# Kernel optimization log

Measured on AMD Instinct MI355X. Metric: run time of the kernel, lower is better.

Reference implementation:

```python
import jax, jax.numpy as jnp
import numpy as np

B, N, K, C, DK, DV, H, W = 16, 5, 5, 512, 128, 128, 16, 16

def setup_inputs() -> dict:
    key = jax.random.key(0)
    k1, k2, k3, k4 = jax.random.split(key, 4)
    return {
        "query_repr": jax.random.normal(k1, (B, C, H, W), dtype=jnp.float32),
        "supports_repr": jax.random.normal(k2, (B, N, K, C, H, W), dtype=jnp.float32),
        "w_qk": jax.random.normal(k3, (DK, C), dtype=jnp.float32) * (C ** -0.5),
        "w_v": jax.random.normal(k4, (DV, C), dtype=jnp.float32) * (C ** -0.5),
    }

def reference(query_repr, supports_repr, w_qk, w_v):
    scale = DK ** -0.5
    # 1x1 convs == per-pixel linear projections
    query_q = jnp.einsum('oc,bchw->bohw', w_qk, query_repr)          # [b,dk,h,w]
    query_v = jnp.einsum('oc,bchw->bohw', w_v, query_repr)           # [b,dv,h,w]
    supports_k = jnp.einsum('oc,bnkchw->bnkohw', w_qk, supports_repr)  # [b,n,k,dk,h,w]
    supports_v = jnp.einsum('oc,bnkchw->bnkohw', w_v, supports_repr)   # [b,n,k,dv,h,w]

    # attention: query pixel (h,w) attends over all support pixels (k,i,j)
    sim = jnp.einsum('bchw,bnkcij->bnhwkij', query_q, supports_k) * scale
    b, n, h, w = sim.shape[:4]
    attn = jax.nn.softmax(sim.reshape(b, n, h, w, -1), axis=-1)
    attn = attn.reshape(b, n, h, w, K, h, w)
    out = jnp.einsum('bnhwkij,bnkcij->bnchw', attn, supports_v)      # [b,n,dv,h,w]

    out = out.reshape(b, n, -1)                                      # [b,n,dv*h*w]
    qv = query_v.reshape(b, 1, -1)                                   # [b,1,dv*h*w]
    euclidean_dist = jnp.sum((qv - out) ** 2, axis=-1) / (h * w)     # [b,n]
    return -euclidean_dist
```

## Files before the change

kernel.cpp:

```cpp
#include <hip/hip_runtime.h>
#include <hip/hip_bf16.h>
#include <stdint.h>

constexpr int Bv = 16, Nv = 5, Kv = 5, Cv = 512, DKv = 128, DVv = 128, HWv = 256;
constexpr int NSUP = Bv * Nv * Kv;
constexpr int NSLAB = NSUP + Bv;

typedef __attribute__((ext_vector_type(8))) short bf16x8;
typedef __attribute__((ext_vector_type(4))) float f32x4;

static __device__ __forceinline__ unsigned short f2b(float x) {
  __hip_bfloat16 h = __float2bfloat16(x);
  return *reinterpret_cast<unsigned short*>(&h);
}

#define SB0() __builtin_amdgcn_sched_barrier(0)
#define BARRIER() __builtin_amdgcn_s_barrier()
#define WAITVM(N) asm volatile("s_waitcnt vmcnt(" #N ")" ::: "memory")
#define WAITLGKM0() asm volatile("s_waitcnt lgkmcnt(0)" ::: "memory")

__global__ __launch_bounds__(256) void prep_kernel(
    const float* __restrict__ query, const float* __restrict__ w_qk,
    const float* __restrict__ w_v, unsigned short* __restrict__ WbF,
    unsigned short* __restrict__ Xb, float* __restrict__ out, int out_n) {
  __shared__ unsigned short lds[64][68];
  const int bid = blockIdx.x;
  const int tid = threadIdx.x;
  if (bid < 64) {
    int gidx = bid * 256 + tid;
    int l = gidx & 63;
    int nb = (gidx >> 6) & 7;
    int ks = (gidx >> 9) & 1;
    int kt = (gidx >> 10) & 7;
    int h = (gidx >> 13) & 1;
    int row = nb * 16 + (l & 15);
    int c0 = kt * 64 + ks * 32 + (l >> 4) * 8;
    const float* src = (h ? w_v : w_qk) + (size_t)row * Cv + c0;
    float4 a = *(const float4*)src;
    float4 b = *(const float4*)(src + 4);
    union { unsigned short u[8]; uint4 v; } t;
    t.u[0] = f2b(a.x); t.u[1] = f2b(a.y); t.u[2] = f2b(a.z); t.u[3] = f2b(a.w);
    t.u[4] = f2b(b.x); t.u[5] = f2b(b.y); t.u[6] = f2b(b.z); t.u[7] = f2b(b.w);
    *(uint4*)(WbF + (size_t)gidx * 8) = t.v;
  } else if (bid < 576) {
    const int blk = bid - 64;
    const int s = NSUP + (blk >> 5);
    const int tq = blk & 31;
    const int cb = tq >> 2, pb = tq & 3;
    const int c0 = cb * 64, p0 = pb * 64;
    const float* __restrict__ X = query + (size_t)(s - NSUP) * Cv * HWv;
#pragma unroll
    for (int r = 0; r < 4; ++r) {
      int cl = (tid >> 4) + r * 16;
      int pl = (tid & 15) * 4;
      float4 v = *(const float4*)(X + (size_t)(c0 + cl) * HWv + p0 + pl);
      ushort4 u;
      u.x = f2b(v.x); u.y = f2b(v.y); u.z = f2b(v.z); u.w = f2b(v.w);
      *(ushort4*)&lds[cl][pl] = u;
    }
    __syncthreads();
    const int pl2 = tid >> 2;
    const int q0 = (tid & 3) * 16;
    union { unsigned short u[16]; uint4 v4[2]; } tmp;
#pragma unroll
    for (int jj = 0; jj < 16; ++jj) {
      int j = (jj + pl2) & 15;
      tmp.u[j] = lds[q0 + j][pl2];
    }
    unsigned short* dst = Xb + ((size_t)s * HWv + p0 + pl2) * Cv + c0 + q0;
    *(uint4*)dst = tmp.v4[0];
    *((uint4*)dst + 1) = tmp.v4[1];
  } else {
    if (tid < out_n) out[tid] = 0.0f;
  }
}

__global__ __launch_bounds__(256, 3) void proj_all_kernel(
    const float* __restrict__ supports, const unsigned short* __restrict__ WbF,
    unsigned short* __restrict__ KbF, unsigned short* __restrict__ VbF,
    const unsigned short* __restrict__ Xb, unsigned short* __restrict__ Qb,
    float* __restrict__ QVf) {
  __shared__ __align__(16) char smem[49152];
  const int bid = blockIdx.x;
  const int t = threadIdx.x;
  const int lane = t & 63, wid = t >> 6;
  const int wr = wid >> 1, wc = wid & 1;
  const int l15 = lane & 15, g = lane >> 4;

  f32x4 acc[2][8] = {};

  if (bid < 1600) {
    const int s = bid >> 2;
    const int pixq = bid & 3;
    float* F0 = (float*)smem;
    float* F1 = (float*)(smem + 16384);
    unsigned short* X0 = (unsigned short*)(smem + 32768);
    unsigned short* X1 = (unsigned short*)(smem + 40960);
    const float* __restrict__ Xs = supports + (size_t)s * Cv * HWv + pixq * 64;

    auto dma = [&](int kt, float* dstF) {
#pragma unroll
      for (int i = 0; i < 4; ++i) {
        const int seg = wid * 4 + i;
        const float* gsrc =
            Xs + (size_t)(kt * 64 + seg * 4 + (lane >> 4)) * HWv + (lane & 15) * 4;
        __builtin_amdgcn_global_load_lds(
            (const __attribute__((address_space(1))) void*)gsrc,
            (__attribute__((address_space(3))) void*)((char*)dstF + seg * 1024),
            16, 0, 0);
      }
    };
    auto stageB = [&](const float* srcF, unsigned short* dstX) {
#pragma unroll
      for (int h2 = 0; h2 < 2; ++h2) {
        const int sidx = h2 * 256 + t;
        const int sslot = sidx >> 6;
        const int row = sidx & 63;
        union { unsigned short u[8]; uint4 q; } pk;
#pragma unroll
        for (int j = 0; j < 8; ++j)
          pk.u[j] = f2b(srcF[(size_t)(sslot * 8 + j) * 64 + row]);
        *(uint4*)((char*)dstX + row * 128 + ((sslot ^ (row & 7)) * 16)) = pk.q;
      }
    };

    dma(0, F0);
    dma(1, F1);
    SB0(); WAITVM(4); SB0(); BARRIER(); SB0();
    stageB(F0, X0);
    WAITLGKM0(); SB0(); BARRIER(); SB0();

    for (int kt = 0; kt < 8; ++kt) {
      const int cur = kt & 1;
      float* Fc = cur ? F1 : F0;
      const unsigned short* Xc = cur ? X1 : X0;
      if (kt < 6) dma(kt + 2, Fc);
#pragma unroll
      for (int ks = 0; ks < 2; ++ks) {
        const int sx = ((ks * 4 + g) ^ (l15 & 7)) * 16;
        bf16x8 A[2], Bf[8];
#pragma unroll
        for (int m = 0; m < 2; ++m)
          A[m] = *(const bf16x8*)((const char*)Xc + (wr * 32 + m * 16 + l15) * 128 + sx);
#pragma unroll
        for (int n = 0; n < 8; ++n) {
          const int h = n >> 2;
          const int nb = wc * 4 + (n & 3);
          Bf[n] = *(const bf16x8*)(
              WbF + (size_t)((((h * 8 + kt) * 2 + ks) * 8 + nb) * 64 + lane) * 8);
        }
#pragma unroll
        for (int m = 0; m < 2; ++m)
#pragma unroll
          for (int n = 0; n < 8; ++n)
            acc[m][n] = __builtin_amdgcn_mfma_f32_16x16x32_bf16(A[m], Bf[n],
                                                                acc[m][n], 0, 0, 0);
      }
      if (kt < 7) {
        SB0();
        if (kt < 6) { WAITVM(4); } else { WAITVM(0); }
        SB0(); BARRIER(); SB0();
        float* Fn = cur ? F0 : F1;
        unsigned short* Xn = cur ? X0 : X1;
        stageB(Fn, Xn);
        WAITLGKM0(); SB0(); BARRIER(); SB0();
      }
    }

    unsigned short* bounce = (unsigned short*)smem;
#pragma unroll
    for (int m = 0; m < 2; ++m) {
      const int pr = wr * 32 + m * 16 + g * 4;
#pragma unroll
      for (int n = 0; n < 4; ++n) {
        const int dk = wc * 64 + n * 16 + l15;
#pragma unroll
        for (int r = 0; r < 4; ++r)
          bounce[(size_t)(pr + r) * 140 + dk] = f2b(acc[m][n][r]);
      }
    }
    __syncthreads();
    {
      unsigned short* Kdst = KbF + ((size_t)s * 4 + pixq) * 8192;
#pragma unroll
      for (int i = 0; i < 4; ++i) {
        const int u = i * 256 + t;
        const int jl15 = u & 15, jg = (u >> 4) & 3, jkc = (u >> 6) & 3,
                  jnc = (u >> 8) & 3;
        const int pixl = jnc * 16 + jl15;
        const int dk = jkc * 32 + jg * 8;
        *(uint4*)(Kdst + (size_t)u * 8) = *(const uint4*)(bounce + (size_t)pixl * 140 + dk);
      }
    }
    __syncthreads();
#pragma unroll
    for (int m = 0; m < 2; ++m) {
      const int pr = wr * 32 + m * 16 + g * 4;
#pragma unroll
      for (int n = 0; n < 4; ++n) {
        const int dv = wc * 64 + n * 16 + l15;
#pragma unroll
        for (int r = 0; r < 4; ++r)
          bounce[(size_t)dv * 72 + pr + r] = f2b(acc[m][4 + n][r]);
      }
    }
    __syncthreads();
    {
      unsigned short* Vdst = VbF + ((size_t)s * 4 + pixq) * 8192;
#pragma unroll
      for (int i = 0; i < 4; ++i) {
        const int u = i * 256 + t;
        const int jl15 = u & 15, jg = (u >> 4) & 3, jd = (u >> 6) & 7,
                  jkc2 = (u >> 9) & 1;
        const int dv = jd * 16 + jl15;
        const int nsl = jkc2 * 32 + jg * 8;
        *(uint4*)(Vdst + (size_t)u * 8) = *(const uint4*)(bounce + (size_t)dv * 72 + nsl);
      }
    }
  } else {
    const int r0 = bid - 1600;
    const int sq = r0 >> 2;
    const int pixq = r0 & 3;
    unsigned short* Xt2 = (unsigned short*)smem;
    const unsigned short* __restrict__ Xq =
        Xb + ((size_t)(NSUP + sq) * HWv + pixq * 64) * Cv;

    auto dmaQ = [&](int kt, int buf) {
#pragma unroll
      for (int i = 0; i < 2; ++i) {
        const int seg = wid * 2 + i;
        const int row = seg * 8 + (lane >> 3);
        const int srcslot = (lane & 7) ^ ((lane >> 3) & 7);
        const unsigned short* gsrc = Xq + (size_t)row * Cv + kt * 64 + srcslot * 8;
        __builtin_amdgcn_global_load_lds(
            (const __attribute__((address_space(1))) void*)gsrc,
            (__attribute__((address_space(3))) void*)((char*)Xt2 + buf * 8192 + seg * 1024),
            16, 0, 0);
      }
    };

    dmaQ(0, 0);
    dmaQ(1, 1);
    SB0(); WAITVM(2); SB0(); BARRIER(); SB0();
    for (int kt = 0; kt < 8; ++kt) {
      if (kt < 6) dmaQ(kt + 2, (kt + 2) & 3);
      const char* Xt = (const char*)Xt2 + (kt & 3) * 8192;
#pragma unroll
      for (int ks = 0; ks < 2; ++ks) {
        const int sx = ((ks * 4 + g) ^ (l15 & 7)) * 16;
        bf16x8 A[2], Bf[8];
#pragma unroll
        for (int m = 0; m < 2; ++m)
          A[m] = *(const bf16x8*)(Xt + (wr * 32 + m * 16 + l15) * 128 + sx);
#pragma unroll
        for (int n = 0; n < 8; ++n) {
          const int h = n >> 2;
          const int nb = wc * 4 + (n & 3);
          Bf[n] = *(const bf16x8*)(
              WbF + (size_t)((((h * 8 + kt) * 2 + ks) * 8 + nb) * 64 + lane) * 8);
        }
#pragma unroll
        for (int m = 0; m < 2; ++m)
#pragma unroll
          for (int n = 0; n < 8; ++n)
            acc[m][n] = __builtin_amdgcn_mfma_f32_16x16x32_bf16(A[m], Bf[n],
                                                                acc[m][n], 0, 0, 0);
      }
      if (kt < 7) {
        SB0();
        if (kt < 6) { WAITVM(2); } else { WAITVM(0); }
        SB0(); BARRIER(); SB0();
      }
    }

#pragma unroll
    for (int m = 0; m < 2; ++m) {
      const int pixr = pixq * 64 + wr * 32 + m * 16 + g * 4;
#pragma unroll
      for (int n = 0; n < 4; ++n) {
        const int oc = wc * 64 + n * 16 + l15;
        unsigned short* p = Qb + ((size_t)sq * HWv + pixr) * DKv + oc;
#pragma unroll
        for (int r = 0; r < 4; ++r) p[(size_t)r * DKv] = f2b(acc[m][n][r]);
      }
#pragma unroll
      for (int n = 0; n < 4; ++n) {
        const int oc = wc * 64 + n * 16 + l15;
        float* p = QVf + ((size_t)sq * HWv + pixr) * DVv + oc;
#pragma unroll
        for (int r = 0; r < 4; ++r) p[(size_t)r * DVv] = acc[m][4 + n][r];
      }
    }
  }
}

__global__ __launch_bounds__(256) void attn_mfma_kernel(
    const unsigned short* __restrict__ KbF, const unsigned short* __restrict__ VbF,
    const unsigned short* __restrict__ Qb, const float* __restrict__ QVf,
    float* __restrict__ out) {
  __shared__ __align__(16) char smem[74784];
  unsigned short* Klds = (unsigned short*)smem;
  unsigned short* Vlds = (unsigned short*)(smem + 32768);
  unsigned short* Plds = (unsigned short*)(smem + 65536);
  float* redbuf = (float*)(smem + 74752);

  const int L = blockIdx.x;
  const int bid = (L & 7) * 40 + (L >> 3);
  const int bn = bid >> 2, qh = bid & 3;
  const int b = bn / Nv;
  const int t = threadIdx.x;
  const int l = t & 63, wid = t >> 6;
  const int l15 = l & 15, g = l >> 4;
  const int qpix0 = qh * 64 + wid * 16;
  constexpr float C2 = 0.08838834764831845f * 1.4426950408889634f;

  bf16x8 qa[4];
#pragma unroll
  for (int kc = 0; kc < 4; ++kc)
    qa[kc] = *(const bf16x8*)(
        Qb + ((size_t)(b * HWv + qpix0 + l15)) * DKv + kc * 32 + g * 8);

  f32x4 oacc[8] = {};
  float mrow[4], lrow[4];
#pragma unroll
  for (int r = 0; r < 4; ++r) { mrow[r] = -3e38f; lrow[r] = 0.0f; }

  unsigned short* Pw = Plds + wid * 16 * 72;

  auto dma = [&](int c, int buf) {
    const int s2 = bn * Kv + (c >> 2);
    const int chunk = c & 3;
    const unsigned short* Kc = KbF + ((size_t)s2 * 4 + chunk) * 8192;
    const unsigned short* Vc = VbF + ((size_t)s2 * 4 + chunk) * 8192;
#pragma unroll
    for (int i = 0; i < 4; ++i) {
      const int seg = wid * 4 + i;
      __builtin_amdgcn_global_load_lds(
          (const __attribute__((address_space(1))) void*)(Kc + (size_t)(seg * 64 + l) * 8),
          (__attribute__((address_space(3))) void*)(Klds + (size_t)buf * 8192 + seg * 512),
          16, 0, 0);
      __builtin_amdgcn_global_load_lds(
          (const __attribute__((address_space(1))) void*)(Vc + (size_t)(seg * 64 + l) * 8),
          (__attribute__((address_space(3))) void*)(Vlds + (size_t)buf * 8192 + seg * 512),
          16, 0, 0);
    }
  };

  dma(0, 0);
  __syncthreads();
  for (int c = 0; c < 20; ++c) {
    const int cur = c & 1;
    if (c < 19) dma(c + 1, cur ^ 1);
    const unsigned short* Kc = Klds + (size_t)cur * 8192;
    const unsigned short* Vc = Vlds + (size_t)cur * 8192;

    f32x4 s4[4];
#pragma unroll
    for (int nc = 0; nc < 4; ++nc) {
      f32x4 sv = {};
#pragma unroll
      for (int kc = 0; kc < 4; ++kc) {
        bf16x8 kf = *(const bf16x8*)(Kc + (size_t)((nc * 4 + kc) * 64 + l) * 8);
        sv = __builtin_amdgcn_mfma_f32_16x16x32_bf16(qa[kc], kf, sv, 0, 0, 0);
      }
      s4[nc] = sv;
    }
    float pm[4];
#pragma unroll
    for (int r = 0; r < 4; ++r) {
      float v = s4[0][r];
#pragma unroll
      for (int nc = 1; nc < 4; ++nc) v = fmaxf(v, s4[nc][r]);
      pm[r] = v;
    }
#pragma unroll
    for (int off = 1; off <= 8; off <<= 1)
#pragma unroll
      for (int r = 0; r < 4; ++r) pm[r] = fmaxf(pm[r], __shfl_xor(pm[r], off));
    float sc[4];
#pragma unroll
    for (int r = 0; r < 4; ++r) {
      float mn = fmaxf(mrow[r], pm[r]);
      sc[r] = exp2f(C2 * (mrow[r] - mn));
      mrow[r] = mn;
      lrow[r] *= sc[r];
    }
#pragma unroll
    for (int d = 0; d < 8; ++d)
#pragma unroll
      for (int r = 0; r < 4; ++r) oacc[d][r] *= sc[r];
#pragma unroll
    for (int nc = 0; nc < 4; ++nc)
#pragma unroll
      for (int r = 0; r < 4; ++r) {
        float p = exp2f(C2 * (s4[nc][r] - mrow[r]));
        lrow[r] += p;
        Pw[(size_t)(g * 4 + r) * 72 + nc * 16 + l15] = f2b(p);
      }
#pragma unroll
    for (int kc2 = 0; kc2 < 2; ++kc2) {
      bf16x8 pa = *(const bf16x8*)(Pw + (size_t)l15 * 72 + kc2 * 32 + g * 8);
#pragma unroll
      for (int d = 0; d < 8; ++d) {
        bf16x8 vf = *(const bf16x8*)(Vc + (size_t)((kc2 * 8 + d) * 64 + l) * 8);
        oacc[d] = __builtin_amdgcn_mfma_f32_16x16x32_bf16(pa, vf, oacc[d], 0, 0, 0);
      }
    }
    __syncthreads();
  }

#pragma unroll
  for (int off = 1; off <= 8; off <<= 1)
#pragma unroll
    for (int r = 0; r < 4; ++r) lrow[r] += __shfl_xor(lrow[r], off);
  float linv[4];
#pragma unroll
  for (int r = 0; r < 4; ++r) linv[r] = 1.0f / lrow[r];

  float part = 0.0f;
#pragma unroll
  for (int d = 0; d < 8; ++d)
#pragma unroll
    for (int r = 0; r < 4; ++r) {
      float o = oacc[d][r] * linv[r];
      float qv = QVf[((size_t)(b * HWv + qpix0 + g * 4 + r)) * DVv + d * 16 + l15];
      float df = qv - o;
      part += df * df;
    }
#pragma unroll
  for (int off = 1; off <= 32; off <<= 1) part += __shfl_xor(part, off);
  if (l == 0) redbuf[wid] = part;
  __syncthreads();
  if (t == 0) {
    float tot = redbuf[0] + redbuf[1] + redbuf[2] + redbuf[3];
    atomicAdd(out + bn, -tot * (1.0f / HWv));
  }
}

extern "C" void kernel_launch(void* const* d_in, const int* in_sizes, int n_in,
                              void* d_out, int out_size, void* d_ws, size_t ws_size,
                              hipStream_t stream) {
  const float* query = (const float*)d_in[0];
  const float* supports = (const float*)d_in[1];
  const float* w_qk = (const float*)d_in[2];
  const float* w_v = (const float*)d_in[3];
  float* out = (float*)d_out;

  const size_t sz_kb = (size_t)NSUP * 4 * 8192 * 2;
  const size_t sz_vb = (size_t)NSUP * 4 * 8192 * 2;
  const size_t sz_qb = (size_t)Bv * HWv * DKv * 2;
  const size_t sz_qvf = (size_t)Bv * HWv * DVv * 4;
  const size_t sz_xb = (size_t)NSLAB * HWv * Cv * 2;
  const size_t sz_wb = (size_t)256 * Cv * 2;

  char* p = (char*)d_ws;
  unsigned short* KbF = (unsigned short*)p;           p += sz_kb;
  unsigned short* VbF = (unsigned short*)p;           p += sz_vb;
  unsigned short* Qb = (unsigned short*)p;            p += sz_qb;
  float* QVf = (float*)p;                             p += sz_qvf;
  unsigned short* Xb = (unsigned short*)p;            p += sz_xb;
  p += sz_wb;
  unsigned short* WbF = (unsigned short*)p;

  prep_kernel<<<577, 256, 0, stream>>>(query, w_qk, w_v, WbF, Xb, out, out_size);
  proj_all_kernel<<<1664, 256, 0, stream>>>(supports, WbF, KbF, VbF, Xb, Qb, QVf);
  attn_mfma_kernel<<<Bv * Nv * 4, 256, 0, stream>>>(KbF, VbF, Qb, QVf, out);
}
```

Measured before the change: 152.8 us.

## Stage support tiles through registers and repartition waves by output head

The support projection path drops the async global-to-LDS fp32 staging buffers. Each thread now loads its fp32 values into registers one k-tile ahead, converts them to bf16 and writes them directly into the swizzled LDS tile, which cuts LDS from 48KB to 32KB. The wave split also changes: each wave now covers all 64 pixels for one head (K or V) and half of the channels, so every B fragment load feeds more MFMAs. The costs are more registers for the prefetched values, and simple vmcnt(0) waits in the query path that may expose load latency.

```diff
diff --git a/kernel.cpp b/kernel.cpp
--- a/kernel.cpp
+++ b/kernel.cpp
@@ -16,7 +16,6 @@
 
 #define SB0() __builtin_amdgcn_sched_barrier(0)
 #define BARRIER() __builtin_amdgcn_s_barrier()
-#define WAITVM(N) asm volatile("s_waitcnt vmcnt(" #N ")" ::: "memory")
 #define WAITLGKM0() asm volatile("s_waitcnt lgkmcnt(0)" ::: "memory")
 
 __global__ __launch_bounds__(256) void prep_kernel(
@@ -80,103 +79,91 @@
     unsigned short* __restrict__ KbF, unsigned short* __restrict__ VbF,
     const unsigned short* __restrict__ Xb, unsigned short* __restrict__ Qb,
     float* __restrict__ QVf) {
-  __shared__ __align__(16) char smem[49152];
+  __shared__ __align__(16) char smem[32768];
   const int bid = blockIdx.x;
   const int t = threadIdx.x;
   const int lane = t & 63, wid = t >> 6;
-  const int wr = wid >> 1, wc = wid & 1;
+  const int wc = wid & 3;
+  const int hsel = wc >> 1;
+  const int nq = wc & 1;
   const int l15 = lane & 15, g = lane >> 4;
 
-  f32x4 acc[2][8] = {};
+  f32x4 acc[4][4] = {};
 
   if (bid < 1600) {
     const int s = bid >> 2;
     const int pixq = bid & 3;
-    float* F0 = (float*)smem;
-    float* F1 = (float*)(smem + 16384);
-    unsigned short* X0 = (unsigned short*)(smem + 32768);
-    unsigned short* X1 = (unsigned short*)(smem + 40960);
+    unsigned short* X0 = (unsigned short*)smem;
+    unsigned short* X1 = (unsigned short*)(smem + 8192);
     const float* __restrict__ Xs = supports + (size_t)s * Cv * HWv + pixq * 64;
-
-    auto dma = [&](int kt, float* dstF) {
-#pragma unroll
-      for (int i = 0; i < 4; ++i) {
-        const int seg = wid * 4 + i;
-        const float* gsrc =
-            Xs + (size_t)(kt * 64 + seg * 4 + (lane >> 4)) * HWv + (lane & 15) * 4;
-        __builtin_amdgcn_global_load_lds(
-            (const __attribute__((address_space(1))) void*)gsrc,
-            (__attribute__((address_space(3))) void*)((char*)dstF + seg * 1024),
-            16, 0, 0);
-      }
+    const int slot0 = wid, slot1 = wid + 4;
+
+    float fst[16];
+    auto aload = [&](int kt) {
+#pragma unroll
+      for (int j = 0; j < 8; ++j)
+        fst[j] = Xs[(size_t)(kt * 64 + slot0 * 8 + j) * HWv + lane];
+#pragma unroll
+      for (int j = 0; j < 8; ++j)
+        fst[8 + j] = Xs[(size_t)(kt * 64 + slot1 * 8 + j) * HWv + lane];
     };
-    auto stageB = [&](const float* srcF, unsigned short* dstX) {
-#pragma unroll
-      for (int h2 = 0; h2 < 2; ++h2) {
-        const int sidx = h2 * 256 + t;
-        const int sslot = sidx >> 6;
-        const int row = sidx & 63;
-        union { unsigned short u[8]; uint4 q; } pk;
-#pragma unroll
-        for (int j = 0; j < 8; ++j)
-          pk.u[j] = f2b(srcF[(size_t)(sslot * 8 + j) * 64 + row]);
-        *(uint4*)((char*)dstX + row * 128 + ((sslot ^ (row & 7)) * 16)) = pk.q;
-      }
+    auto awrite = [&](unsigned short* dstX) {
+      union { unsigned short u[8]; uint4 q; } pk;
+#pragma unroll
+      for (int j = 0; j < 8; ++j) pk.u[j] = f2b(fst[j]);
+      *(uint4*)((char*)dstX + lane * 128 + ((slot0 ^ (lane & 7)) * 16)) = pk.q;
+#pragma unroll
+      for (int j = 0; j < 8; ++j) pk.u[j] = f2b(fst[8 + j]);
+      *(uint4*)((char*)dstX + lane * 128 + ((slot1 ^ (lane & 7)) * 16)) = pk.q;
     };
 
-    dma(0, F0);
-    dma(1, F1);
-    SB0(); WAITVM(4); SB0(); BARRIER(); SB0();
-    stageB(F0, X0);
+    aload(0);
+    awrite(X0);
     WAITLGKM0(); SB0(); BARRIER(); SB0();
 
     for (int kt = 0; kt < 8; ++kt) {
       const int cur = kt & 1;
-      float* Fc = cur ? F1 : F0;
       const unsigned short* Xc = cur ? X1 : X0;
-      if (kt < 6) dma(kt + 2, Fc);
+      unsigned short* Xn = cur ? X0 : X1;
+      if (kt < 7) aload(kt + 1);
+      SB0();
 #pragma unroll
       for (int ks = 0; ks < 2; ++ks) {
         const int sx = ((ks * 4 + g) ^ (l15 & 7)) * 16;
-        bf16x8 A[2], Bf[8];
-#pragma unroll
-        for (int m = 0; m < 2; ++m)
-          A[m] = *(const bf16x8*)((const char*)Xc + (wr * 32 + m * 16 + l15) * 128 + sx);
-#pragma unroll
-        for (int n = 0; n < 8; ++n) {
-          const int h = n >> 2;
-          const int nb = wc * 4 + (n & 3);
+        bf16x8 A[4], Bf[4];
+#pragma unroll
+        for (int m = 0; m < 4; ++m)
+          A[m] = *(const bf16x8*)((const char*)Xc + (m * 16 + l15) * 128 + sx);
+#pragma unroll
+        for (int n = 0; n < 4; ++n)
           Bf[n] = *(const bf16x8*)(
-              WbF + (size_t)((((h * 8 + kt) * 2 + ks) * 8 + nb) * 64 + lane) * 8);
-        }
-#pragma unroll
-        for (int m = 0; m < 2; ++m)
-#pragma unroll
-          for (int n = 0; n < 8; ++n)
+              WbF + (size_t)((((hsel * 8 + kt) * 2 + ks) * 8 + nq * 4 + n) * 64 + lane) * 8);
+#pragma unroll
+        for (int m = 0; m < 4; ++m)
+#pragma unroll
+          for (int n = 0; n < 4; ++n)
             acc[m][n] = __builtin_amdgcn_mfma_f32_16x16x32_bf16(A[m], Bf[n],
                                                                 acc[m][n], 0, 0, 0);
       }
       if (kt < 7) {
-        SB0();
-        if (kt < 6) { WAITVM(4); } else { WAITVM(0); }
-        SB0(); BARRIER(); SB0();
-        float* Fn = cur ? F0 : F1;
-        unsigned short* Xn = cur ? X0 : X1;
-        stageB(Fn, Xn);
+        awrite(Xn);
         WAITLGKM0(); SB0(); BARRIER(); SB0();
       }
     }
 
+    __syncthreads();
     unsigned short* bounce = (unsigned short*)smem;
-#pragma unroll
-    for (int m = 0; m < 2; ++m) {
-      const int pr = wr * 32 + m * 16 + g * 4;
-#pragma unroll
-      for (int n = 0; n < 4; ++n) {
-        const int dk = wc * 64 + n * 16 + l15;
-#pragma unroll
-        for (int r = 0; r < 4; ++r)
-          bounce[(size_t)(pr + r) * 140 + dk] = f2b(acc[m][n][r]);
+    if (hsel == 0) {
+#pragma unroll
+      for (int m = 0; m < 4; ++m) {
+        const int pr = m * 16 + g * 4;
+#pragma unroll
+        for (int n = 0; n < 4; ++n) {
+          const int dk = nq * 64 + n * 16 + l15;
+#pragma unroll
+          for (int r = 0; r < 4; ++r)
+            bounce[(size_t)(pr + r) * 140 + dk] = f2b(acc[m][n][r]);
+        }
       }
     }
     __syncthreads();
@@ -193,15 +180,17 @@
       }
     }
     __syncthreads();
-#pragma unroll
-    for (int m = 0; m < 2; ++m) {
-      const int pr = wr * 32 + m * 16 + g * 4;
-#pragma unroll
-      for (int n = 0; n < 4; ++n) {
-        const int dv = wc * 64 + n * 16 + l15;
-#pragma unroll
-        for (int r = 0; r < 4; ++r)
-          bounce[(size_t)dv * 72 + pr + r] = f2b(acc[m][4 + n][r]);
+    if (hsel == 1) {
+#pragma unroll
+      for (int m = 0; m < 4; ++m) {
+        const int pr = m * 16 + g * 4;
+#pragma unroll
+        for (int n = 0; n < 4; ++n) {
+          const int dv = nq * 64 + n * 16 + l15;
+#pragma unroll
+          for (int r = 0; r < 4; ++r)
+            bounce[(size_t)dv * 72 + pr + r] = f2b(acc[m][n][r]);
+        }
       }
     }
     __syncthreads();
@@ -241,54 +230,51 @@
 
     dmaQ(0, 0);
     dmaQ(1, 1);
-    SB0(); WAITVM(2); SB0(); BARRIER(); SB0();
+    asm volatile("s_waitcnt vmcnt(2)" ::: "memory");
+    SB0(); BARRIER(); SB0();
     for (int kt = 0; kt < 8; ++kt) {
       if (kt < 6) dmaQ(kt + 2, (kt + 2) & 3);
       const char* Xt = (const char*)Xt2 + (kt & 3) * 8192;
 #pragma unroll
       for (int ks = 0; ks < 2; ++ks) {
         const int sx = ((ks * 4 + g) ^ (l15 & 7)) * 16;
-        bf16x8 A[2], Bf[8];
-#pragma unroll
-        for (int m = 0; m < 2; ++m)
-          A[m] = *(const bf16x8*)(Xt + (wr * 32 + m * 16 + l15) * 128 + sx);
-#pragma unroll
-        for (int n = 0; n < 8; ++n) {
-          const int h = n >> 2;
-          const int nb = wc * 4 + (n & 3);
+        bf16x8 A[4], Bf[4];
+#pragma unroll
+        for (int m = 0; m < 4; ++m)
+          A[m] = *(const bf16x8*)(Xt + (m * 16 + l15) * 128 + sx);
+#pragma unroll
+        for (int n = 0; n < 4; ++n)
           Bf[n] = *(const bf16x8*)(
-              WbF + (size_t)((((h * 8 + kt) * 2 + ks) * 8 + nb) * 64 + lane) * 8);
-        }
-#pragma unroll
-        for (int m = 0; m < 2; ++m)
-#pragma unroll
-          for (int n = 0; n < 8; ++n)
+              WbF + (size_t)((((hsel * 8 + kt) * 2 + ks) * 8 + nq * 4 + n) * 64 + lane) * 8);
+#pragma unroll
+        for (int m = 0; m < 4; ++m)
+#pragma unroll
+          for (int n = 0; n < 4; ++n)
             acc[m][n] = __builtin_amdgcn_mfma_f32_16x16x32_bf16(A[m], Bf[n],
                                                                 acc[m][n], 0, 0, 0);
       }
       if (kt < 7) {
         SB0();
-        if (kt < 6) { WAITVM(2); } else { WAITVM(0); }
+        asm volatile("s_waitcnt vmcnt(0)" ::: "memory");
         SB0(); BARRIER(); SB0();
       }
     }
 
 #pragma unroll
-    for (int m = 0; m < 2; ++m) {
-      const int pixr = pixq * 64 + wr * 32 + m * 16 + g * 4;
+    for (int m = 0; m < 4; ++m) {
+      const int pixr = pixq * 64 + m * 16 + g * 4;
 #pragma unroll
       for (int n = 0; n < 4; ++n) {
-        const int oc = wc * 64 + n * 16 + l15;
-        unsigned short* p = Qb + ((size_t)sq * HWv + pixr) * DKv + oc;
-#pragma unroll
-        for (int r = 0; r < 4; ++r) p[(size_t)r * DKv] = f2b(acc[m][n][r]);
-      }
-#pragma unroll
-      for (int n = 0; n < 4; ++n) {
-        const int oc = wc * 64 + n * 16 + l15;
-        float* p = QVf + ((size_t)sq * HWv + pixr) * DVv + oc;
-#pragma unroll
-        for (int r = 0; r < 4; ++r) p[(size_t)r * DVv] = acc[m][4 + n][r];
+        const int oc = nq * 64 + n * 16 + l15;
+        if (hsel == 0) {
+          unsigned short* p = Qb + ((size_t)sq * HWv + pixr) * DKv + oc;
+#pragma unroll
+          for (int r = 0; r < 4; ++r) p[(size_t)r * DKv] = f2b(acc[m][n][r]);
+        } else {
+          float* p = QVf + ((size_t)sq * HWv + pixr) * DVv + oc;
+#pragma unroll
+          for (int r = 0; r < 4; ++r) p[(size_t)r * DVv] = acc[m][n][r];
+        }
       }
     }
   }
```

Result: faster. 145.3 us (-4.9%).
